# Optimization experiments

Measured on AMD Instinct MI355X. Metric: run time of the kernel, lower is better.

Reference implementation:

```python
import jax, jax.numpy as jnp
import numpy as np

N = 16384   # total nodes
G = 256     # graphs in batch
E0 = 131072 # random edges (self loops appended, matching PyG add_self_loops=True)
IN = 256
H = 8       # heads
F = 64      # per-head out dim (h1=h2=h3)


def setup_inputs() -> dict:
    key = jax.random.key(0)
    ks = jax.random.split(key, 40)
    nrm = lambda k, shape, s=0.05: jax.random.normal(k, shape, jnp.float32) * s
    x = jax.random.normal(ks[0], (N, IN), jnp.float32)
    src0 = jax.random.randint(ks[1], (E0,), 0, N)
    dst0 = jax.random.randint(ks[2], (E0,), 0, N)
    loop = jnp.arange(N)
    inp = dict(
        x=x,
        edge_src=jnp.concatenate([src0, loop]),
        edge_dst=jnp.concatenate([dst0, loop]),
        batch=jnp.repeat(jnp.arange(G), N // G),
    )
    dims_in = [IN, H * F, H * F]
    norm_dim = [H * F, H * F, F]
    bias_dim = [H * F, H * F, F]  # conv3 concat=False -> bias size F
    ki = 3
    for i in range(3):
        d = dims_in[i]
        inp[f'Wl{i+1}'] = nrm(ks[ki], (d, H * F)); ki += 1
        inp[f'Wr{i+1}'] = nrm(ks[ki], (d, H * F)); ki += 1
        inp[f'att{i+1}'] = nrm(ks[ki], (H, F)); ki += 1
        inp[f'b{i+1}'] = nrm(ks[ki], (bias_dim[i],)); ki += 1
        inp[f'gnw{i+1}'] = jnp.ones((norm_dim[i],), jnp.float32)
        inp[f'gnb{i+1}'] = jnp.zeros((norm_dim[i],), jnp.float32)
        inp[f'gnm{i+1}'] = jnp.ones((norm_dim[i],), jnp.float32)
    inp['Wlin'] = nrm(ks[ki], (F, 2)); ki += 1
    inp['blin'] = jnp.zeros((2,), jnp.float32)
    return inp


def _gatv2(x, Wl, Wr, att, b, src, dst, concat):
    # GATv2Conv (PyG defaults: share_weights=False, negative_slope=0.2), eval mode (no dropout)
    n = x.shape[0]
    Hh, Ff = att.shape
    xl = (x @ Wl).reshape(n, Hh, Ff)
    xr = (x @ Wr).reshape(n, Hh, Ff)
    m = xl[src] + xr[dst]                      # [E, H, F]
    e = jnp.where(m > 0, m, 0.2 * m)           # leaky_relu
    logit = jnp.einsum('ehf,hf->eh', e, att)   # [E, H]
    lmax = jax.ops.segment_max(logit, dst, num_segments=n)
    lmax = jnp.where(jnp.isneginf(lmax), 0.0, lmax)
    p = jnp.exp(logit - lmax[dst])
    den = jax.ops.segment_sum(p, dst, num_segments=n)
    alpha = p / (den[dst] + 1e-16)             # PyG softmax eps
    out = jax.ops.segment_sum(alpha[:, :, None] * xl[src], dst, num_segments=n)
    out = out.reshape(n, Hh * Ff) if concat else out.mean(axis=1)
    return out + b


def _graphnorm(x, w, b, ms, batch, g):
    cnt = jax.ops.segment_sum(jnp.ones((x.shape[0],), x.dtype), batch, num_segments=g)[:, None]
    mean = jax.ops.segment_sum(x, batch, num_segments=g) / cnt
    xc = x - ms * mean[batch]
    var = jax.ops.segment_sum(xc * xc, batch, num_segments=g) / cnt
    return w * xc / jnp.sqrt(var[batch] + 1e-5) + b


def reference(x, edge_src, edge_dst, batch,
              Wl1, Wr1, att1, b1, gnw1, gnb1, gnm1,
              Wl2, Wr2, att2, b2, gnw2, gnb2, gnm2,
              Wl3, Wr3, att3, b3, gnw3, gnb3, gnm3,
              Wlin, blin):
    h = jax.nn.relu(_graphnorm(_gatv2(x, Wl1, Wr1, att1, b1, edge_src, edge_dst, True), gnw1, gnb1, gnm1, batch, G))
    h = jax.nn.relu(_graphnorm(_gatv2(h, Wl2, Wr2, att2, b2, edge_src, edge_dst, True), gnw2, gnb2, gnm2, batch, G))
    h = jax.nn.relu(_graphnorm(_gatv2(h, Wl3, Wr3, att3, b3, edge_src, edge_dst, False), gnw3, gnb3, gnm3, batch, G))
    cnt = jax.ops.segment_sum(jnp.ones((h.shape[0],), h.dtype), batch, num_segments=G)[:, None]
    pooled = jax.ops.segment_sum(h, batch, num_segments=G) / cnt  # global_mean_pool
    return pooled @ Wlin + blin
```

## Files before the change

### kernel.cpp

```cpp
#include <hip/hip_runtime.h>
#include <hip/hip_bf16.h>
#include <stdint.h>
#include <string.h>

#define NNODES 16384
#define GIN 256
#define NG 64
#define NGRAPH 256
#define FDIM 64
#define CDIM 512

typedef __attribute__((ext_vector_type(8))) short bf16x8;
typedef __attribute__((ext_vector_type(4))) float f32x4;

__device__ __forceinline__ float bf2f(unsigned short u){
  union { unsigned int i; float f; } w; w.i = ((unsigned int)u) << 16; return w.f;
}

__device__ __forceinline__ void unpk(unsigned int u, float& lo, float& hi){
  union { unsigned int i; float f; } a, b;
  a.i = u << 16; b.i = u & 0xffff0000u;
  lo = a.f; hi = b.f;
}

union PK8 { __hip_bfloat16 h[8]; uint4 v; };

__device__ __forceinline__ void async16(const void* g, void* l){
  __builtin_amdgcn_global_load_lds(
      (const __attribute__((address_space(1))) unsigned int*)g,
      (__attribute__((address_space(3))) unsigned int*)l, 16, 0, 0);
}

__global__ void k_detect(const unsigned short* __restrict__ x, int* __restrict__ flag){
  int lane = threadIdx.x;
  int bad = 0;
  #pragma unroll
  for (int j = 0; j < 4; j++){
    float f = bf2f(x[lane*4 + j]);
    if (!(fabsf(f) < 1e4f)) bad++;
  }
  #pragma unroll
  for (int o = 32; o; o >>= 1) bad += __shfl_down(bad, o);
  if (lane == 0) *flag = (bad > 16) ? 1 : 0;
}

struct CArgs {
  const void* p[17];
  int cum[18];
};

__global__ void k_convert(CArgs a, const int* __restrict__ flag, float* __restrict__ dst, int total){
  int isf32 = *flag;
  for (int idx = blockIdx.x*blockDim.x + threadIdx.x; idx < total; idx += gridDim.x*blockDim.x){
    int seg = 0;
    while (idx >= a.cum[seg+1]) seg++;
    int off = idx - a.cum[seg];
    float v;
    if (isf32) v = ((const float*)a.p[seg])[off];
    else       v = bf2f(((const unsigned short*)a.p[seg])[off]);
    dst[idx] = v;
  }
}

__global__ void k_xconv(const void* __restrict__ xin, const int* __restrict__ flag,
                        __hip_bfloat16* __restrict__ xbf, int* __restrict__ deg, int total){
  int isf32 = *flag;
  for (int idx = blockIdx.x*blockDim.x + threadIdx.x; idx < total; idx += gridDim.x*blockDim.x){
    if (idx < NNODES) deg[idx] = 0;
    float v;
    if (isf32) v = ((const float*)xin)[idx];
    else       v = bf2f(((const unsigned short*)xin)[idx]);
    xbf[idx] = __float2bfloat16(v);
  }
}

struct TArgs {
  const void* W[6];
  __hip_bfloat16* Wt[6];
  int K[6];
};

__global__ void k_transpose_all(TArgs t, const int* __restrict__ flag){
  int isf32 = *flag;
  int seg = blockIdx.z;
  int K = t.K[seg];
  int n0 = blockIdx.x*32, k0 = blockIdx.y*32;
  if (k0 >= K) return;
  const void* W = t.W[seg];
  __hip_bfloat16* Wt = t.Wt[seg];
  __shared__ float tl[32][33];
  for (int r = threadIdx.y; r < 32; r += 8){
    size_t idx = (size_t)(k0 + r)*CDIM + n0 + threadIdx.x;
    tl[r][threadIdx.x] = isf32 ? ((const float*)W)[idx] : bf2f(((const unsigned short*)W)[idx]);
  }
  __syncthreads();
  for (int r = threadIdx.y; r < 32; r += 8)
    Wt[(size_t)(n0 + r)*K + k0 + threadIdx.x] = __float2bfloat16(tl[threadIdx.x][r]);
}

__global__ void k_count(const int* __restrict__ edst, int E, int* __restrict__ deg){
  int e = blockIdx.x*blockDim.x + threadIdx.x;
  if (e < E) atomicAdd(&deg[edst[e]], 1);
}

__global__ void k_scan(const int* __restrict__ deg, int* __restrict__ off, int* __restrict__ cur){
  __shared__ int ss[256];
  int t = threadIdx.x;
  int base = t * 64;
  int s = 0;
  for (int j = 0; j < 64; j++) s += deg[base + j];
  ss[t] = s;
  __syncthreads();
  for (int o = 1; o < 256; o <<= 1){
    int v = 0;
    if (t >= o) v = ss[t - o];
    __syncthreads();
    if (t >= o) ss[t] += v;
    __syncthreads();
  }
  int run = ss[t] - s;
  for (int j = 0; j < 64; j++){
    int i = base + j;
    off[i] = run;
    cur[i] = run;
    run += deg[i];
  }
  if (t == 255) off[NNODES] = run;
}

__global__ void k_fill(const int* __restrict__ esrc, const int* __restrict__ edst, int E,
                       int* __restrict__ cur, int* __restrict__ srcs){
  int e = blockIdx.x*blockDim.x + threadIdx.x;
  if (e < E){
    int pos = atomicAdd(&cur[edst[e]], 1);
    srcs[pos] = esrc[e];
  }
}

#define GBAR  do { asm volatile("" ::: "memory"); __builtin_amdgcn_s_barrier(); asm volatile("" ::: "memory"); } while(0)

#define PHASE(BUF, MH, NH, LA, LB, SBUF, SISB, SUNIT, ST, DOVM)                                   \
  { if (LA){ _Pragma("unroll") for (int ko_=0;ko_<2;ko_++)                                        \
               _Pragma("unroll") for (int ii_=0;ii_<4;ii_++) Afr[ko_][ii_]=rdA(BUF,MH,ii_,ko_); } \
    if (LB){ _Pragma("unroll") for (int ko_=0;ko_<2;ko_++)                                        \
               _Pragma("unroll") for (int jj_=0;jj_<2;jj_++) Bfr[ko_][jj_]=rdB(BUF,NH,jj_,ko_); } \
    stage(SBUF,SISB,SUNIT,ST);                                                                    \
    if (DOVM) asm volatile("s_waitcnt vmcnt(4)" ::: "memory");                                    \
    GBAR;                                                                                         \
    __builtin_amdgcn_s_setprio(1);                                                                \
    _Pragma("unroll") for (int ii_=0;ii_<4;ii_++)                                                 \
      _Pragma("unroll") for (int jj_=0;jj_<2;jj_++)                                               \
        _Pragma("unroll") for (int ko_=0;ko_<2;ko_++)                                             \
          acc[(MH)*4+ii_][(NH)*2+jj_] = __builtin_amdgcn_mfma_f32_16x16x32_bf16(                  \
              Afr[ko_][ii_], Bfr[ko_][jj_], acc[(MH)*4+ii_][(NH)*2+jj_], 0, 0, 0);                \
    __builtin_amdgcn_s_setprio(0);                                                                \
    GBAR; }

__global__ __launch_bounds__(512, 2) void k_gemm256(
    const __hip_bfloat16* __restrict__ A,
    const __hip_bfloat16* __restrict__ Wtl, const __hip_bfloat16* __restrict__ Wtr,
    __hip_bfloat16* __restrict__ Cl, __hip_bfloat16* __restrict__ Cr, int K){
  const __hip_bfloat16* Wt = blockIdx.z ? Wtr : Wtl;
  __hip_bfloat16*       C  = blockIdx.z ? Cr  : Cl;
  __shared__ __align__(128) char lds[131072];
  const int tid = threadIdx.x;
  const int w = tid >> 6, lane = tid & 63;
  const int wm = w >> 2, wn = w & 3;
  const int l16 = lane & 15, c4 = lane >> 4;
  const int row0 = blockIdx.x * 256, col0 = blockIdx.y * 256;
  const int NT = K >> 6;

  f32x4 acc[8][4];
  #pragma unroll
  for (int i = 0; i < 8; i++)
    #pragma unroll
    for (int j = 0; j < 4; j++) acc[i][j] = (f32x4){0.f,0.f,0.f,0.f};

  bf16x8 Afr[2][4];
  bf16x8 Bfr[2][2];

  const __hip_bfloat16* Ag = A  + (size_t)row0 * K;
  const __hip_bfloat16* Bg = Wt + (size_t)col0 * K;

  auto stage = [&](int buf, int isB, int unit, int t){
    int k0 = (t < NT ? t : t - NT) << 6;
    #pragma unroll
    for (int j = 0; j < 2; j++){
      int u0 = (w*2 + j) * 8;
      int uidx = u0 + (lane >> 3);
      int row, rs;
      if (!isB){ row = (uidx & 63) | ((uidx & 64) << 1) | (unit << 6);
                 rs  = (u0   & 63) | ((u0   & 64) << 1) | (unit << 6); }
      else     { row = ((uidx & 96) << 1) | (uidx & 31) | (unit << 5);
                 rs  = ((u0   & 96) << 1) | (u0   & 31) | (unit << 5); }
      int chunk = (lane & 7) ^ (uidx & 7);
      const __hip_bfloat16* gp = (isB ? Bg : Ag) + (size_t)row * K + k0 + chunk * 8;
      async16(gp, lds + (isB ? 65536 : 0) + buf * 32768 + rs * 128);
    }
  };

  auto rdA = [&](int buf, int mh, int ii, int ko)->bf16x8{
    int row = wm*128 + mh*64 + ii*16 + l16;
    int chunk = ((ko<<2) + c4) ^ (l16 & 7);
    return *(const bf16x8*)(lds + buf*32768 + row*128 + chunk*16);
  };
  auto rdB = [&](int buf, int nh, int jj, int ko)->bf16x8{
    int row = wn*64 + nh*32 + jj*16 + l16;
    int chunk = ((ko<<2) + c4) ^ (l16 & 7);
    return *(const bf16x8*)(lds + 65536 + buf*32768 + row*128 + chunk*16);
  };

  stage(0,0,0,0); stage(0,1,1,0); stage(0,0,1,0); stage(0,1,0,0);
  stage(1,0,0,1); stage(1,1,1,1);
  asm volatile("s_waitcnt vmcnt(4)" ::: "memory");
  GBAR;

  for (int t = 0; t < NT; t += 2){
    PHASE(0, 0, 0, 1, 1, 1, 0, 1, t+1, 0)
    PHASE(0, 0, 1, 0, 1, 1, 1, 0, t+1, 0)
    PHASE(0, 1, 1, 1, 0, 0, 0, 0, t+2, 0)
    PHASE(0, 1, 0, 0, 1, 0, 1, 1, t+2, 1)
    PHASE(1, 0, 0, 1, 1, 0, 0, 1, t+2, 0)
    PHASE(1, 0, 1, 0, 1, 0, 1, 0, t+2, 0)
    PHASE(1, 1, 1, 1, 0, 1, 0, 0, t+3, 0)
    PHASE(1, 1, 0, 0, 1, 1, 1, 1, t+3, 1)
  }

  asm volatile("s_waitcnt vmcnt(0)" ::: "memory");
  GBAR;
  {
    __hip_bfloat16* ct = (__hip_bfloat16*)lds;
    #pragma unroll
    for (int i = 0; i < 8; i++)
      #pragma unroll
      for (int j = 0; j < 4; j++)
        #pragma unroll
        for (int r = 0; r < 4; r++){
          int rl = wm*128 + i*16 + c4*4 + r;
          int cl = wn*64  + j*16 + l16;
          ct[rl*256 + cl] = __float2bfloat16(acc[i][j][r]);
        }
  }
  GBAR;
  #pragma unroll
  for (int s = 0; s < 16; s++){
    int seg = s*512 + tid;
    int rl = seg >> 5, ch = seg & 31;
    uint4 v = *(const uint4*)(lds + rl*512 + ch*16);
    *(uint4*)((char*)(C + (size_t)(row0 + rl)*CDIM + col0) + ch*16) = v;
  }
}

template<int CONCAT>
__global__ __launch_bounds__(256) void k_fused_attn(
    const __hip_bfloat16* __restrict__ XL, const __hip_bfloat16* __restrict__ XR,
    const float* __restrict__ att,
    const int* __restrict__ off, const int* __restrict__ srcs,
    const float* __restrict__ bias, __hip_bfloat16* __restrict__ OUT){
  int wave = threadIdx.x >> 6, lane = threadIdx.x & 63;
  int d = blockIdx.x * 4 + wave;
  if (d >= NNODES) return;

  uint4 xru = *(const uint4*)((const char*)XR + ((size_t)d*CDIM + lane*8)*2);
  float xr[8];
  unpk(xru.x, xr[0], xr[1]); unpk(xru.y, xr[2], xr[3]);
  unpk(xru.z, xr[4], xr[5]); unpk(xru.w, xr[6], xr[7]);
  const float4* atp = (const float4*)(att + lane*8);
  float4 at0 = atp[0], at1 = atp[1];
  float at[8] = {at0.x, at0.y, at0.z, at0.w, at1.x, at1.y, at1.z, at1.w};

  float acc[8];
  #pragma unroll
  for (int j = 0; j < 8; j++) acc[j] = 0.f;
  float den = 0.f;

  int beg = off[d], end = off[d+1];

  auto leaky = [](float m){ return fmaxf(m, 0.2f*m); };

  for (int i = beg; i < end; i += 4){
    int n = end - i;
    int s0 = srcs[i];
    int s1 = n > 1 ? srcs[i+1] : s0;
    int s2 = n > 2 ? srcs[i+2] : s0;
    int s3 = n > 3 ? srcs[i+3] : s0;
    uint4 rw[4];
    rw[0] = *(const uint4*)((const char*)XL + ((size_t)s0*CDIM + lane*8)*2);
    rw[1] = *(const uint4*)((const char*)XL + ((size_t)s1*CDIM + lane*8)*2);
    rw[2] = *(const uint4*)((const char*)XL + ((size_t)s2*CDIM + lane*8)*2);
    rw[3] = *(const uint4*)((const char*)XL + ((size_t)s3*CDIM + lane*8)*2);

    #pragma unroll
    for (int e = 0; e < 4; e++){
      if (e < n){
        float xv[8];
        unpk(rw[e].x, xv[0], xv[1]);
        unpk(rw[e].y, xv[2], xv[3]);
        unpk(rw[e].z, xv[4], xv[5]);
        unpk(rw[e].w, xv[6], xv[7]);
        float v = 0.f;
        #pragma unroll
        for (int j = 0; j < 8; j++) v = fmaf(leaky(xv[j] + xr[j]), at[j], v);
        v += __shfl_xor(v, 1); v += __shfl_xor(v, 2); v += __shfl_xor(v, 4);
        float p = expf(v);
        den += p;
        #pragma unroll
        for (int j = 0; j < 8; j++) acc[j] = fmaf(p, xv[j], acc[j]);
      }
    }
  }

  float inv = 1.f / (den + 1e-16f);
  const float4* bp = (const float4*)(bias + (CONCAT ? lane*8 : (lane & 7)*8));

  if (CONCAT){
    float4 b0v = bp[0], b1v = bp[1];
    float bb[8] = {b0v.x, b0v.y, b0v.z, b0v.w, b1v.x, b1v.y, b1v.z, b1v.w};
    PK8 pk;
    #pragma unroll
    for (int j = 0; j < 8; j++)
      pk.h[j] = __float2bfloat16(acc[j]*inv + bb[j]);
    *(uint4*)((char*)OUT + ((size_t)d*CDIM + lane*8)*2) = pk.v;
  } else {
    float r[8];
    #pragma unroll
    for (int j = 0; j < 8; j++) r[j] = acc[j] * inv;
    #pragma unroll
    for (int o = 8; o < 64; o <<= 1)
      #pragma unroll
      for (int j = 0; j < 8; j++) r[j] += __shfl_xor(r[j], o);
    if (lane < 8){
      float4 b0v = bp[0], b1v = bp[1];
      float bb[8] = {b0v.x, b0v.y, b0v.z, b0v.w, b1v.x, b1v.y, b1v.z, b1v.w};
      PK8 pk;
      #pragma unroll
      for (int j = 0; j < 8; j++)
        pk.h[j] = __float2bfloat16(r[j]*0.125f + bb[j]);
      *(uint4*)((char*)OUT + ((size_t)d*FDIM + lane*8)*2) = pk.v;
    }
  }
}

__global__ void k_graphnorm_relu(const __hip_bfloat16* __restrict__ X, const float* __restrict__ w,
    const float* __restrict__ b, const float* __restrict__ ms,
    __hip_bfloat16* __restrict__ Y, int C){
  int g = blockIdx.x;
  int c = threadIdx.x;
  const __hip_bfloat16* xg = X + (size_t)g * NG * C + c;
  __hip_bfloat16* yg = Y + (size_t)g * NG * C + c;
  float v[NG];
  float s1 = 0.f, s2 = 0.f;
  #pragma unroll
  for (int i = 0; i < NG; i++){
    v[i] = __bfloat162float(xg[(size_t)i*C]);
    s1 += v[i]; s2 += v[i]*v[i];
  }
  float mean = s1 * (1.f/NG);
  float m = ms[c];
  float var = s2 * (1.f/NG) - 2.f*m*mean*mean + m*m*mean*mean;
  float inv = rsqrtf(var + 1e-5f);
  float ww = w[c], bb = b[c];
  #pragma unroll
  for (int i = 0; i < NG; i++){
    float y = fmaf(ww * (v[i] - m*mean), inv, bb);
    yg[(size_t)i*C] = __float2bfloat16(y > 0.f ? y : 0.f);
  }
}

__global__ void k_pool_linear(const __hip_bfloat16* __restrict__ H, const float* __restrict__ Wlin,
    const float* __restrict__ blin, void* out, const int* __restrict__ flag){
  int g = blockIdx.x, c = threadIdx.x;
  float s = 0.f;
  for (int i = 0; i < NG; i++) s += __bfloat162float(H[(long)(g*NG + i)*FDIM + c]);
  float pooled = s * (1.f/NG);
  float v0 = pooled * Wlin[c*2 + 0];
  float v1 = pooled * Wlin[c*2 + 1];
  #pragma unroll
  for (int o = 32; o; o >>= 1){ v0 += __shfl_down(v0, o); v1 += __shfl_down(v1, o); }
  if (c == 0){
    float o0 = v0 + blin[0], o1 = v1 + blin[1];
    if (*flag){
      ((float*)out)[g*2 + 0] = o0;
      ((float*)out)[g*2 + 1] = o1;
    } else {
      ((__hip_bfloat16*)out)[g*2 + 0] = __float2bfloat16(o0);
      ((__hip_bfloat16*)out)[g*2 + 1] = __float2bfloat16(o1);
    }
  }
}

extern "C" void kernel_launch(void* const* d_in, const int* in_sizes, int n_in,
                              void* d_out, int out_size, void* d_ws, size_t ws_size,
                              hipStream_t stream){
  const int N = NNODES;
  const int E = in_sizes[1];

  const int* esrc = (const int*)d_in[1];
  const int* edst = (const int*)d_in[2];

  char* ws = (char*)d_ws;
  size_t cursor_b = 0;
  auto alloc = [&](size_t bytes)->char*{
    char* p = ws + cursor_b;
    cursor_b += (bytes + 255) & ~size_t(255);
    return p;
  };

  int* flag = (int*)alloc(256);

  static const int convIdx[17] = {6,7,8,9,10, 13,14,15,16,17, 20,21,22,23,24, 25,26};
  CArgs ca;
  int cums[18]; cums[0] = 0;
  for (int i = 0; i < 17; i++){
    ca.p[i] = d_in[convIdx[i]];
    cums[i+1] = cums[i] + in_sizes[convIdx[i]];
  }
  memcpy(ca.cum, cums, sizeof(cums));
  int totalConv = cums[17];

  float* conv = (float*)alloc((size_t)totalConv * 4);
  const float* fw[17];
  for (int i = 0; i < 17; i++) fw[i] = conv + cums[i];

  __hip_bfloat16* XLbf  = (__hip_bfloat16*)alloc((size_t)N * CDIM * 2);
  __hip_bfloat16* XRbf  = (__hip_bfloat16*)alloc((size_t)N * CDIM * 2);
  __hip_bfloat16* OUTbf = (__hip_bfloat16*)alloc((size_t)N * CDIM * 2);
  __hip_bfloat16* OUT3  = (__hip_bfloat16*)alloc((size_t)N * FDIM * 2);
  __hip_bfloat16* HBbf  = (__hip_bfloat16*)alloc((size_t)N * CDIM * 2);
  __hip_bfloat16* xbf   = (__hip_bfloat16*)alloc((size_t)N * GIN * 2);
  __hip_bfloat16* Wt[6];
  Wt[0] = (__hip_bfloat16*)alloc((size_t)CDIM * GIN * 2);
  Wt[1] = (__hip_bfloat16*)alloc((size_t)CDIM * GIN * 2);
  Wt[2] = (__hip_bfloat16*)alloc((size_t)CDIM * CDIM * 2);
  Wt[3] = (__hip_bfloat16*)alloc((size_t)CDIM * CDIM * 2);
  Wt[4] = (__hip_bfloat16*)alloc((size_t)CDIM * CDIM * 2);
  Wt[5] = (__hip_bfloat16*)alloc((size_t)CDIM * CDIM * 2);
  int* deg  = (int*)alloc((size_t)N * 4);
  int* off  = (int*)alloc((size_t)(N + 1) * 4);
  int* cur  = (int*)alloc((size_t)N * 4);
  int* srcs = (int*)alloc((size_t)E * 4);

  k_detect<<<1, 64, 0, stream>>>((const unsigned short*)d_in[0], flag);
  k_convert<<<32, 256, 0, stream>>>(ca, flag, conv, totalConv);
  k_xconv<<<2048, 256, 0, stream>>>(d_in[0], flag, xbf, deg, N * GIN);
  {
    TArgs ta;
    const void* Ws[6] = {d_in[4], d_in[5], d_in[11], d_in[12], d_in[18], d_in[19]};
    const int   Ks[6] = {GIN, GIN, CDIM, CDIM, CDIM, CDIM};
    for (int i = 0; i < 6; i++){ ta.W[i] = Ws[i]; ta.Wt[i] = Wt[i]; ta.K[i] = Ks[i]; }
    k_transpose_all<<<dim3(CDIM/32, CDIM/32, 6), dim3(32, 8), 0, stream>>>(ta, flag);
  }

  k_count<<<(E + 255)/256, 256, 0, stream>>>(edst, E, deg);
  k_scan<<<1, 256, 0, stream>>>(deg, off, cur);
  k_fill<<<(E + 255)/256, 256, 0, stream>>>(esrc, edst, E, cur, srcs);

  const float* att_[3] = {fw[0],  fw[5],  fw[10]};
  const float* b_[3]   = {fw[1],  fw[6],  fw[11]};
  const float* gw_[3]  = {fw[2],  fw[7],  fw[12]};
  const float* gb_[3]  = {fw[3],  fw[8],  fw[13]};
  const float* gm_[3]  = {fw[4],  fw[9],  fw[14]};

  const __hip_bfloat16* inbuf = xbf;
  int K = GIN;
  for (int layer = 0; layer < 3; layer++){
    k_gemm256<<<dim3(N/256, CDIM/256, 2), 512, 0, stream>>>(
        inbuf, Wt[layer*2], Wt[layer*2 + 1], XLbf, XRbf, K);
    if (layer < 2){
      k_fused_attn<1><<<N/4, 256, 0, stream>>>(XLbf, XRbf, att_[layer], off, srcs, b_[layer], OUTbf);
      k_graphnorm_relu<<<NGRAPH, CDIM, 0, stream>>>(OUTbf, gw_[layer], gb_[layer], gm_[layer], HBbf, CDIM);
    } else {
      k_fused_attn<0><<<N/4, 256, 0, stream>>>(XLbf, XRbf, att_[layer], off, srcs, b_[layer], OUT3);
      k_graphnorm_relu<<<NGRAPH, FDIM, 0, stream>>>(OUT3, gw_[layer], gb_[layer], gm_[layer], HBbf, FDIM);
    }
    inbuf = HBbf;
    K = CDIM;
  }

  k_pool_linear<<<NGRAPH, 64, 0, stream>>>(HBbf, fw[15], fw[16], d_out, flag);
}
```

Baseline: 324.1 us.

## Fold dtype detection into kernels, fuse degree count, double-buffer attention gathers

Removes the separate dtype-detection kernel: each kernel now samples the input itself to decide fp32 vs bf16. Degree zeroing moves into the convert kernel, and edge counting is fused into the x-conversion kernel. This cuts two launches and a serial dependency. The scan is vectorised with int4 loads and stores, and the attention kernel software-pipelines its neighbour-row gathers with two register buffers so the next loads are in flight during compute. Risks are redundant per-thread detection reads and extra register pressure in the attention kernel.

Result: no change. 322.3 us (-0.6%).

```diff
diff --git a/kernel.cpp b/kernel.cpp
--- a/kernel.cpp
+++ b/kernel.cpp
@@ -31,17 +31,14 @@
       (__attribute__((address_space(3))) unsigned int*)l, 16, 0, 0);
 }
 
-__global__ void k_detect(const unsigned short* __restrict__ x, int* __restrict__ flag){
-  int lane = threadIdx.x;
+__device__ __forceinline__ int is_f32(const unsigned short* __restrict__ x){
   int bad = 0;
   #pragma unroll
-  for (int j = 0; j < 4; j++){
-    float f = bf2f(x[lane*4 + j]);
+  for (int j = 0; j < 64; j++){
+    float f = bf2f(x[j*4]);
     if (!(fabsf(f) < 1e4f)) bad++;
   }
-  #pragma unroll
-  for (int o = 32; o; o >>= 1) bad += __shfl_down(bad, o);
-  if (lane == 0) *flag = (bad > 16) ? 1 : 0;
+  return bad > 4;
 }
 
 struct CArgs {
@@ -49,9 +46,12 @@
   int cum[18];
 };
 
-__global__ void k_convert(CArgs a, const int* __restrict__ flag, float* __restrict__ dst, int total){
-  int isf32 = *flag;
-  for (int idx = blockIdx.x*blockDim.x + threadIdx.x; idx < total; idx += gridDim.x*blockDim.x){
+__global__ void k_convert(CArgs a, const unsigned short* __restrict__ x,
+                          float* __restrict__ dst, int total, int* __restrict__ deg){
+  int isf32 = is_f32(x);
+  int totAll = total + NNODES;
+  for (int idx = blockIdx.x*blockDim.x + threadIdx.x; idx < totAll; idx += gridDim.x*blockDim.x){
+    if (idx >= total){ deg[idx - total] = 0; continue; }
     int seg = 0;
     while (idx >= a.cum[seg+1]) seg++;
     int off = idx - a.cum[seg];
@@ -62,16 +62,18 @@
   }
 }
 
-__global__ void k_xconv(const void* __restrict__ xin, const int* __restrict__ flag,
-                        __hip_bfloat16* __restrict__ xbf, int* __restrict__ deg, int total){
-  int isf32 = *flag;
+__global__ void k_xconv_count(const void* __restrict__ xin,
+                              __hip_bfloat16* __restrict__ xbf, int total,
+                              const int* __restrict__ edst, int E, int* __restrict__ deg){
+  int isf32 = is_f32((const unsigned short*)xin);
   for (int idx = blockIdx.x*blockDim.x + threadIdx.x; idx < total; idx += gridDim.x*blockDim.x){
-    if (idx < NNODES) deg[idx] = 0;
     float v;
     if (isf32) v = ((const float*)xin)[idx];
     else       v = bf2f(((const unsigned short*)xin)[idx]);
     xbf[idx] = __float2bfloat16(v);
   }
+  for (int e = blockIdx.x*blockDim.x + threadIdx.x; e < E; e += gridDim.x*blockDim.x)
+    atomicAdd(&deg[edst[e]], 1);
 }
 
 struct TArgs {
@@ -80,8 +82,8 @@
   int K[6];
 };
 
-__global__ void k_transpose_all(TArgs t, const int* __restrict__ flag){
-  int isf32 = *flag;
+__global__ void k_transpose_all(TArgs t, const unsigned short* __restrict__ x){
+  int isf32 = is_f32(x);
   int seg = blockIdx.z;
   int K = t.K[seg];
   int n0 = blockIdx.x*32, k0 = blockIdx.y*32;
@@ -98,17 +100,17 @@
     Wt[(size_t)(n0 + r)*K + k0 + threadIdx.x] = __float2bfloat16(tl[threadIdx.x][r]);
 }
 
-__global__ void k_count(const int* __restrict__ edst, int E, int* __restrict__ deg){
-  int e = blockIdx.x*blockDim.x + threadIdx.x;
-  if (e < E) atomicAdd(&deg[edst[e]], 1);
-}
-
 __global__ void k_scan(const int* __restrict__ deg, int* __restrict__ off, int* __restrict__ cur){
   __shared__ int ss[256];
   int t = threadIdx.x;
-  int base = t * 64;
+  const int4* d4 = (const int4*)(deg + t*64);
+  int4 buf[16];
   int s = 0;
-  for (int j = 0; j < 64; j++) s += deg[base + j];
+  #pragma unroll
+  for (int j = 0; j < 16; j++){
+    buf[j] = d4[j];
+    s += buf[j].x + buf[j].y + buf[j].z + buf[j].w;
+  }
   ss[t] = s;
   __syncthreads();
   for (int o = 1; o < 256; o <<= 1){
@@ -119,11 +121,16 @@
     __syncthreads();
   }
   int run = ss[t] - s;
-  for (int j = 0; j < 64; j++){
-    int i = base + j;
-    off[i] = run;
-    cur[i] = run;
-    run += deg[i];
+  int4* o4 = (int4*)(off + t*64);
+  int4* c4 = (int4*)(cur + t*64);
+  #pragma unroll
+  for (int j = 0; j < 16; j++){
+    int4 v;
+    v.x = run; run += buf[j].x;
+    v.y = run; run += buf[j].y;
+    v.z = run; run += buf[j].z;
+    v.w = run; run += buf[j].w;
+    o4[j] = v; c4[j] = v;
   }
   if (t == 255) off[NNODES] = run;
 }
@@ -278,18 +285,21 @@
 
   auto leaky = [](float m){ return fmaxf(m, 0.2f*m); };
 
-  for (int i = beg; i < end; i += 4){
+  uint4 rwA[4], rwB[4];
+
+  auto ldgth = [&](int i, uint4* rw){
     int n = end - i;
     int s0 = srcs[i];
     int s1 = n > 1 ? srcs[i+1] : s0;
     int s2 = n > 2 ? srcs[i+2] : s0;
     int s3 = n > 3 ? srcs[i+3] : s0;
-    uint4 rw[4];
     rw[0] = *(const uint4*)((const char*)XL + ((size_t)s0*CDIM + lane*8)*2);
     rw[1] = *(const uint4*)((const char*)XL + ((size_t)s1*CDIM + lane*8)*2);
     rw[2] = *(const uint4*)((const char*)XL + ((size_t)s2*CDIM + lane*8)*2);
     rw[3] = *(const uint4*)((const char*)XL + ((size_t)s3*CDIM + lane*8)*2);
-
+  };
+
+  auto compute = [&](const uint4* rw, int n){
     #pragma unroll
     for (int e = 0; e < 4; e++){
       if (e < n){
@@ -308,6 +318,20 @@
         for (int j = 0; j < 8; j++) acc[j] = fmaf(p, xv[j], acc[j]);
       }
     }
+  };
+
+  ldgth(beg, rwA);
+  int i = beg;
+  while (true){
+    int iB = i + 4;
+    if (iB >= end){ compute(rwA, end - i); break; }
+    ldgth(iB, rwB);
+    compute(rwA, 4);
+    int iA = iB + 4;
+    if (iA >= end){ compute(rwB, end - iB); break; }
+    ldgth(iA, rwA);
+    compute(rwB, 4);
+    i = iA;
   }
 
   float inv = 1.f / (den + 1e-16f);
@@ -368,7 +392,7 @@
 }
 
 __global__ void k_pool_linear(const __hip_bfloat16* __restrict__ H, const float* __restrict__ Wlin,
-    const float* __restrict__ blin, void* out, const int* __restrict__ flag){
+    const float* __restrict__ blin, void* out, const unsigned short* __restrict__ x){
   int g = blockIdx.x, c = threadIdx.x;
   float s = 0.f;
   for (int i = 0; i < NG; i++) s += __bfloat162float(H[(long)(g*NG + i)*FDIM + c]);
@@ -379,7 +403,7 @@
   for (int o = 32; o; o >>= 1){ v0 += __shfl_down(v0, o); v1 += __shfl_down(v1, o); }
   if (c == 0){
     float o0 = v0 + blin[0], o1 = v1 + blin[1];
-    if (*flag){
+    if (is_f32(x)){
       ((float*)out)[g*2 + 0] = o0;
       ((float*)out)[g*2 + 1] = o1;
     } else {
@@ -397,6 +421,7 @@
 
   const int* esrc = (const int*)d_in[1];
   const int* edst = (const int*)d_in[2];
+  const unsigned short* xus = (const unsigned short*)d_in[0];
 
   char* ws = (char*)d_ws;
   size_t cursor_b = 0;
@@ -405,8 +430,6 @@
     cursor_b += (bytes + 255) & ~size_t(255);
     return p;
   };
-
-  int* flag = (int*)alloc(256);
 
   static const int convIdx[17] = {6,7,8,9,10, 13,14,15,16,17, 20,21,22,23,24, 25,26};
   CArgs ca;
@@ -440,18 +463,16 @@
   int* cur  = (int*)alloc((size_t)N * 4);
   int* srcs = (int*)alloc((size_t)E * 4);
 
-  k_detect<<<1, 64, 0, stream>>>((const unsigned short*)d_in[0], flag);
-  k_convert<<<32, 256, 0, stream>>>(ca, flag, conv, totalConv);
-  k_xconv<<<2048, 256, 0, stream>>>(d_in[0], flag, xbf, deg, N * GIN);
+  k_convert<<<32, 256, 0, stream>>>(ca, xus, conv, totalConv, deg);
+  k_xconv_count<<<2048, 256, 0, stream>>>(d_in[0], xbf, N * GIN, edst, E, deg);
   {
     TArgs ta;
     const void* Ws[6] = {d_in[4], d_in[5], d_in[11], d_in[12], d_in[18], d_in[19]};
     const int   Ks[6] = {GIN, GIN, CDIM, CDIM, CDIM, CDIM};
     for (int i = 0; i < 6; i++){ ta.W[i] = Ws[i]; ta.Wt[i] = Wt[i]; ta.K[i] = Ks[i]; }
-    k_transpose_all<<<dim3(CDIM/32, CDIM/32, 6), dim3(32, 8), 0, stream>>>(ta, flag);
-  }
-
-  k_count<<<(E + 255)/256, 256, 0, stream>>>(edst, E, deg);
+    k_transpose_all<<<dim3(CDIM/32, CDIM/32, 6), dim3(32, 8), 0, stream>>>(ta, xus);
+  }
+
   k_scan<<<1, 256, 0, stream>>>(deg, off, cur);
   k_fill<<<(E + 255)/256, 256, 0, stream>>>(esrc, edst, E, cur, srcs);
 
@@ -477,5 +498,5 @@
     K = CDIM;
   }
 
-  k_pool_linear<<<NGRAPH, 64, 0, stream>>>(HBbf, fw[15], fw[16], d_out, flag);
-}
+  k_pool_linear<<<NGRAPH, 64, 0, stream>>>(HBbf, fw[15], fw[16], d_out, xus);
+}
```
